# Optimization experiments

Measured on AMD Instinct MI355X. Metric: run time of the kernel, lower is better.

The kernel has to match this reference:

```python
import jax, jax.numpy as jnp
import numpy as np

B, Q, K, D, H = 4, 2048, 2048, 512, 8
DH = D // H
MASK_VAL = -1e6


def setup_inputs() -> dict:
    key = jax.random.key(0)
    ks = jax.random.split(key, 8)
    queries = jax.random.normal(ks[0], (B, Q, D), dtype=jnp.float32)
    keys = jax.random.normal(ks[1], (B, K, D), dtype=jnp.float32)
    values = jax.random.normal(ks[2], (B, K, D), dtype=jnp.float32)
    valid_lens = jax.random.randint(ks[3], (B,), 1, K + 1, dtype=jnp.int32)
    # torch nn.Linear weights: shape [out_features, in_features], y = x @ W.T
    s = 1.0 / np.sqrt(D)
    W_q = jax.random.uniform(ks[4], (D, D), jnp.float32, -s, s)
    W_k = jax.random.uniform(ks[5], (D, D), jnp.float32, -s, s)
    W_v = jax.random.uniform(ks[6], (D, D), jnp.float32, -s, s)
    W_o = jax.random.uniform(ks[7], (D, D), jnp.float32, -s, s)
    return {"queries": queries, "keys": keys, "values": values,
            "valid_lens": valid_lens, "W_q": W_q, "W_k": W_k,
            "W_v": W_v, "W_o": W_o}


def _split_heads(x):
    # [B, S, D] -> [B, H, S, DH]
    b, s, _ = x.shape
    return x.reshape(b, s, H, DH).transpose(0, 2, 1, 3)


def reference(queries, keys, values, valid_lens, W_q, W_k, W_v, W_o):
    q = _split_heads(queries @ W_q.T)   # [B,H,Q,DH]
    k = _split_heads(keys @ W_k.T)      # [B,H,K,DH]
    v = _split_heads(values @ W_v.T)    # [B,H,K,DH]
    scores = jnp.einsum("bhqd,bhkd->bhqk", q, k) / jnp.sqrt(jnp.float32(DH))
    # padding mask: key position < valid_len[b], broadcast over heads & queries
    mask = jnp.arange(K)[None, None, None, :] < valid_lens[:, None, None, None]
    scores = jnp.where(mask, scores, MASK_VAL)
    attn = jax.nn.softmax(scores, axis=-1)  # dropout=eval/no-op
    out = jnp.einsum("bhqk,bhkd->bhqd", attn, v)
    out = out.transpose(0, 2, 1, 3).reshape(queries.shape[0], q.shape[2], D)
    return out @ W_o.T
```

## Files before the change

### kernel.cpp

```cpp
#include <hip/hip_runtime.h>
#include <cstdint>
#include <cstddef>

#define BB  4
#define QQ  2048
#define SK  2048
#define DD  512
#define HH  8
#define DHH 64
#define CS  8
#define ZMAX 4

typedef __bf16 bf16;
typedef bf16  bf16x8 __attribute__((ext_vector_type(8)));
typedef bf16  bf16x4 __attribute__((ext_vector_type(4)));
typedef float f32x4  __attribute__((ext_vector_type(4)));
typedef _Float16 f16;
typedef f16   f16x4 __attribute__((ext_vector_type(4)));
typedef f16   f16x8 __attribute__((ext_vector_type(8)));

__device__ __forceinline__ void async16(void* lds, const void* g) {
  __builtin_amdgcn_global_load_lds(
      (const __attribute__((address_space(1))) unsigned int*)g,
      (__attribute__((address_space(3))) unsigned int*)lds, 16, 0, 0);
}

__device__ __forceinline__ uint32_t pk2(float lo, float hi) {
  return __builtin_amdgcn_perm(__builtin_bit_cast(uint32_t, hi),
                               __builtin_bit_cast(uint32_t, lo), 0x07060302u);
}

__global__ __launch_bounds__(256) void cvt_all(
    const float* __restrict__ q, const float* __restrict__ k,
    const float* __restrict__ v, const float* __restrict__ w0,
    const float* __restrict__ w1, const float* __restrict__ w2,
    const float* __restrict__ w3, bf16* __restrict__ dq,
    bf16* __restrict__ dk, bf16* __restrict__ dv, bf16* __restrict__ dw0,
    bf16* __restrict__ dw1, bf16* __restrict__ dw2, bf16* __restrict__ dw3,
    int nx4, int nw4) {
  const int y = blockIdx.y;
  const float* s;
  bf16* d;
  int n4;
  if (y < 3) {
    n4 = nx4; s = y == 0 ? q : y == 1 ? k : v;
    d = y == 0 ? dq : y == 1 ? dk : dv;
  } else {
    n4 = nw4;
    s = y == 3 ? w0 : y == 4 ? w1 : y == 5 ? w2 : w3;
    d = y == 3 ? dw0 : y == 4 ? dw1 : y == 5 ? dw2 : dw3;
  }
  int i = blockIdx.x * 256 + threadIdx.x;
  if (i < n4) {
    float4 vv = ((const float4*)s)[i];
    bf16x4 o;
    o[0] = (bf16)vv.x; o[1] = (bf16)vv.y; o[2] = (bf16)vv.z; o[3] = (bf16)vv.w;
    ((bf16x4*)d)[i] = o;
  }
}

template <int MT, typename EpiF>
__device__ __forceinline__ void gemm_body(
    const bf16* __restrict__ A, const bf16* __restrict__ B,
    int tM, int tN, EpiF epi_fn) {
  __shared__ __align__(16) bf16 lA[2][MT * 32 * 64];
  __shared__ __align__(16) bf16 lB[2][128 * 64];
  const int tid  = threadIdx.x;
  const int l    = tid & 63;
  const int w    = tid >> 6;
  const int lrow = l & 15, lq = l >> 4;
  const int wm = (w >> 1) * (MT * 16), wn = (w & 1) * 64;

  auto stage = [&](int kt, int buf) {
#pragma unroll
    for (int j = 0; j < MT; ++j) {
      int c = j * 256 + tid, row = c >> 3, gcc = (c & 7) ^ (row & 7);
      async16(&lA[buf][c * 8], &A[(size_t)(tM + row) * DD + kt + gcc * 8]);
    }
#pragma unroll
    for (int j = 0; j < 4; ++j) {
      int c = j * 256 + tid, row = c >> 3, gcc = (c & 7) ^ (row & 7);
      async16(&lB[buf][c * 8], &B[(size_t)(tN + row) * DD + kt + gcc * 8]);
    }
  };

  f32x4 acc[MT][4] = {};
  stage(0, 0);
  for (int it = 0; it < 8; ++it) {
    __syncthreads();
    if (it + 1 < 8) stage((it + 1) * 64, (it + 1) & 1);
    const bf16* bufA = lA[it & 1];
    const bf16* bufB = lB[it & 1];
#pragma unroll
    for (int ks = 0; ks < 2; ++ks) {
      bf16x8 af[MT], bfr[4];
#pragma unroll
      for (int mt = 0; mt < MT; ++mt) {
        int row = wm + mt * 16 + lrow;
        int chunk = row * 8 + ((ks * 4 + lq) ^ (lrow & 7));
        af[mt] = *(const bf16x8*)&bufA[chunk * 8];
      }
#pragma unroll
      for (int nt = 0; nt < 4; ++nt) {
        int row = wn + nt * 16 + lrow;
        int chunk = row * 8 + ((ks * 4 + lq) ^ (lrow & 7));
        bfr[nt] = *(const bf16x8*)&bufB[chunk * 8];
      }
#pragma unroll
      for (int mt = 0; mt < MT; ++mt)
#pragma unroll
        for (int nt = 0; nt < 4; ++nt)
          acc[mt][nt] = __builtin_amdgcn_mfma_f32_16x16x32_bf16(
              af[mt], bfr[nt], acc[mt][nt], 0, 0, 0);
    }
  }

#pragma unroll
  for (int mt = 0; mt < MT; ++mt)
#pragma unroll
    for (int nt = 0; nt < 4; ++nt) {
      int row0 = tM + wm + mt * 16 + lq * 4;
      int col  = tN + wn + nt * 16 + lrow;
      epi_fn(acc[mt][nt], row0, col);
    }
}

__global__ __launch_bounds__(256, 2) void proj3(
    const bf16* __restrict__ xq, const bf16* __restrict__ wq, bf16* __restrict__ qh,
    const bf16* __restrict__ xk, const bf16* __restrict__ wk, bf16* __restrict__ kh,
    const bf16* __restrict__ xv, const bf16* __restrict__ wv, bf16* __restrict__ vt,
    float qscale) {
  const int z = blockIdx.y, x = blockIdx.x;
  if (z < 2) {
    const bf16* A  = z == 0 ? wq : wk;
    const bf16* B  = z == 0 ? xq : xk;
    bf16* Cout     = z == 0 ? qh : kh;
    const float scale = z == 0 ? qscale : 1.0f;
    int tM = (x & 3) * 128, tN = (x >> 2) * 128;
    gemm_body<4>(A, B, tM, tN, [&](const f32x4& a, int row0, int col) {
      int b2 = col >> 11, s = col & 2047;
      int h2 = row0 >> 6, dh0 = row0 & 63;
      bf16x4 o;
#pragma unroll
      for (int r = 0; r < 4; ++r) o[r] = (bf16)(a[r] * scale);
      *(bf16x4*)&Cout[((size_t)(b2 * HH + h2) * QQ + s) * DHH + dh0] = o;
    });
  } else {
    int tM = (x >> 2) * 128, tN = (x & 3) * 128;
    gemm_body<4>(xv, wv, tM, tN, [&](const f32x4& a, int row0, int col) {
      int b2 = row0 >> 11, s0 = row0 & 2047;
      int h2 = col >> 6,  dh = col & 63;
      int tile = s0 >> 6, kk = s0 & 63;
      int g = kk >> 4, a2 = (kk >> 2) & 3;
      int idx0 = ((g >> 1) * 4 + a2) * 8 + (g & 1) * 4;
      bf16x4 o;
#pragma unroll
      for (int r = 0; r < 4; ++r) o[r] = (bf16)a[r];
      *(bf16x4*)&vt[((size_t)(b2 * HH + h2) * DHH + dh) * SK + tile * 64 + idx0] = o;
    });
  }
}

__global__ __launch_bounds__(256, 2) void proj_o(
    const bf16* __restrict__ wo, const bf16* __restrict__ ao,
    float* __restrict__ Cout) {
  const int x = blockIdx.x;
  int tM = (x & 7) * 64, tN = (x >> 3) * 128;
  gemm_body<2>(wo, ao, tM, tN, [&](const f32x4& a, int row0, int col) {
    *(float4*)&Cout[(size_t)col * DD + row0] = *(const float4*)&a;
  });
}

__global__ __launch_bounds__(256, 4) void attn_split(
    const bf16* __restrict__ qh, const bf16* __restrict__ kh,
    const bf16* __restrict__ vt, const int* __restrict__ valid_lens,
    f16* __restrict__ opart, float* __restrict__ lpart) {
  __shared__ __align__(16) bf16 lK[2][64 * 64];
  __shared__ __align__(16) bf16 lV[2][64 * 64];
  const int tid  = threadIdx.x;
  const int l    = tid & 63;
  const int w    = tid >> 6;
  const int lrow = l & 15, lq = l >> 4;
  const int rx   = lrow & 7;
  const int bh = blockIdx.x;
  const int b = bh >> 3;
  const int qt = blockIdx.y, z = blockIdx.z;
  const int vl  = valid_lens[b];
  const int nkt = (vl + 63) >> 6;
  const int kt0 = z * CS;
  const int kt1 = min(nkt, kt0 + CS);
  const size_t pbase = ((size_t)bh * 16 + qt) * ZMAX + z;
  float* lout = lpart + pbase * 128;
  f16*   oout = opart + pbase * 8192;

  if (kt0 >= kt1) {
    if (tid < 128) lout[tid] = 0.f;
    return;
  }

  const int q0 = qt * 128 + w * 32;
  const bf16* qbase = qh + (size_t)bh * QQ * DHH;
  const bf16* kbase = kh + (size_t)bh * SK * DHH;
  const bf16* vbase = vt + (size_t)bh * DHH * SK;

  bf16x8 qf[2][2];
#pragma unroll
  for (int g = 0; g < 2; ++g)
#pragma unroll
    for (int ks = 0; ks < 2; ++ks)
      qf[g][ks] = *(const bf16x8*)
          &qbase[(size_t)(q0 + g * 16 + lrow) * DHH + ks * 32 + lq * 8];

  auto stageKV = [&](int k0, int buf) {
#pragma unroll
    for (int j = 0; j < 2; ++j) {
      int c = j * 256 + tid, row = c >> 3, gcc = (c & 7) ^ (row & 7);
      async16(&lK[buf][c * 8], &kbase[(size_t)(k0 + row) * DHH + gcc * 8]);
    }
#pragma unroll
    for (int j = 0; j < 2; ++j) {
      int c = j * 256 + tid, row = c >> 3, gcc = (c & 7) ^ (row & 7);
      async16(&lV[buf][c * 8], &vbase[(size_t)row * SK + k0 + gcc * 8]);
    }
  };

  f32x4 acc[2][4] = {};
  float rs[2] = {0.f, 0.f};

  stageKV(kt0 * 64, kt0 & 1);
  for (int kt = kt0; kt < kt1; ++kt) {
    __syncthreads();
    if (kt + 1 < kt1) stageKV((kt + 1) * 64, (kt + 1) & 1);
    const bf16* bufK = lK[kt & 1];
    const bf16* bufV = lV[kt & 1];
    const int k0 = kt * 64;

    f32x4 s[2][4] = {};
#pragma unroll
    for (int ks = 0; ks < 2; ++ks) {
#pragma unroll
      for (int t = 0; t < 4; ++t) {
        int row = t * 16 + lrow;
        int chunkc = row * 8 + ((ks * 4 + lq) ^ rx);
        bf16x8 kf = *(const bf16x8*)&bufK[chunkc * 8];
#pragma unroll
        for (int g = 0; g < 2; ++g)
          s[g][t] = __builtin_amdgcn_mfma_f32_16x16x32_bf16(
              kf, qf[g][ks], s[g][t], 0, 0, 0);
      }
    }

    if (vl < k0 + 64) {
#pragma unroll
      for (int t = 0; t < 4; ++t) {
        int kb = k0 + t * 16 + lq * 4;
#pragma unroll
        for (int r = 0; r < 4; ++r)
          if (kb + r >= vl) { s[0][t][r] = -1e30f; s[1][t][r] = -1e30f; }
      }
    }

#pragma unroll
    for (int g = 0; g < 2; ++g)
#pragma unroll
      for (int t = 0; t < 4; ++t)
#pragma unroll
        for (int r = 0; r < 4; ++r) {
          float p = __builtin_amdgcn_exp2f(s[g][t][r]);
          rs[g] += p;
          s[g][t][r] = p;
        }

#pragma unroll
    for (int p2 = 0; p2 < 2; ++p2) {
      union { bf16x8 v; uint32_t u[4]; } pb[2];
#pragma unroll
      for (int g = 0; g < 2; ++g) {
        pb[g].u[0] = pk2(s[g][2 * p2][0], s[g][2 * p2][1]);
        pb[g].u[1] = pk2(s[g][2 * p2][2], s[g][2 * p2][3]);
        pb[g].u[2] = pk2(s[g][2 * p2 + 1][0], s[g][2 * p2 + 1][1]);
        pb[g].u[3] = pk2(s[g][2 * p2 + 1][2], s[g][2 * p2 + 1][3]);
      }
      int cc = (p2 * 4 + lq) ^ rx;
#pragma unroll
      for (int mt = 0; mt < 4; ++mt) {
        int row = mt * 16 + lrow;
        bf16x8 vf = *(const bf16x8*)&bufV[(row * 8 + cc) * 8];
#pragma unroll
        for (int g = 0; g < 2; ++g)
          acc[g][mt] = __builtin_amdgcn_mfma_f32_16x16x32_bf16(
              vf, pb[g].v, acc[g][mt], 0, 0, 0);
      }
    }
  }

#pragma unroll
  for (int g = 0; g < 2; ++g) {
    rs[g] += __shfl_xor(rs[g], 16);
    rs[g] += __shfl_xor(rs[g], 32);
    if (lq == 0) lout[w * 32 + g * 16 + lrow] = rs[g];
  }

#pragma unroll
  for (int g = 0; g < 2; ++g)
#pragma unroll
    for (int mt = 0; mt < 4; ++mt) {
      f16x4 o;
#pragma unroll
      for (int r = 0; r < 4; ++r) o[r] = (f16)acc[g][mt][r];
      *(f16x4*)&oout[(w * 32 + g * 16 + lrow) * 64 + mt * 16 + lq * 4] = o;
    }
}

__global__ __launch_bounds__(256) void attn_combine(
    const f16* __restrict__ opart, const float* __restrict__ lpart,
    bf16* __restrict__ ao) {
  const int bh = blockIdx.x, qt = blockIdx.y;
  const int b = bh >> 3, h = bh & 7;
  const size_t base = ((size_t)bh * 16 + qt) * ZMAX;
  const int t = threadIdx.x, q = t >> 1, ds = (t & 1) * 32;
  float O[32] = {};
  float lsum = 0.f;
#pragma unroll
  for (int z = 0; z < ZMAX; ++z) {
    float lz = lpart[(base + z) * 128 + q];
    if (lz != 0.f) {
      lsum += lz;
      const f16x8* p = (const f16x8*)&opart[(base + z) * 8192 + q * 64 + ds];
#pragma unroll
      for (int j = 0; j < 4; ++j) {
        f16x8 a = p[j];
#pragma unroll
        for (int r = 0; r < 8; ++r) O[j * 8 + r] += (float)a[r];
      }
    }
  }
  float inv = 1.0f / lsum;
  bf16* dst = &ao[((size_t)(b * QQ + qt * 128 + q)) * DD + h * DHH + ds];
#pragma unroll
  for (int j = 0; j < 4; ++j) {
    bf16x8 o;
#pragma unroll
    for (int r = 0; r < 8; ++r) o[r] = (bf16)(O[j * 8 + r] * inv);
    *(bf16x8*)(dst + j * 8) = o;
  }
}

extern "C" void kernel_launch(void* const* d_in, const int* in_sizes, int n_in,
                              void* d_out, int out_size, void* d_ws, size_t ws_size,
                              hipStream_t stream) {
  const float* queries    = (const float*)d_in[0];
  const float* keys       = (const float*)d_in[1];
  const float* values     = (const float*)d_in[2];
  const int*   valid_lens = (const int*)d_in[3];
  const float* W_q = (const float*)d_in[4];
  const float* W_k = (const float*)d_in[5];
  const float* W_v = (const float*)d_in[6];
  const float* W_o = (const float*)d_in[7];

  const size_t NX = (size_t)BB * QQ * DD;
  const size_t NW = (size_t)DD * DD;

  bf16* xq = (bf16*)d_ws;
  bf16* xk = xq + NX;
  bf16* xv = xk + NX;
  bf16* wq = xv + NX;
  bf16* wk = wq + NW;
  bf16* wv = wk + NW;
  bf16* wo = wv + NW;
  bf16* qh = wo + NW;
  bf16* kh = qh + NX;
  bf16* vt = kh + NX;
  f16*  opart = (f16*)(vt + NX);
  float* lpart = (float*)(opart + (size_t)32 * 16 * ZMAX * 8192);
  bf16* ao = xq;

  dim3 blk(256);
  cvt_all<<<dim3(NX / 1024, 7), blk, 0, stream>>>(
      queries, keys, values, W_q, W_k, W_v, W_o,
      xq, xk, xv, wq, wk, wv, wo, (int)(NX / 4), (int)(NW / 4));

  const float qscale = 0.125f * 1.44269504088896340736f;
  proj3<<<dim3(256, 3), blk, 0, stream>>>(xq, wq, qh, xk, wk, kh, xv, wv, vt,
                                          qscale);

  attn_split<<<dim3(BB * HH, QQ / 128, ZMAX), blk, 0, stream>>>(
      qh, kh, vt, valid_lens, opart, lpart);
  attn_combine<<<dim3(BB * HH, QQ / 128), blk, 0, stream>>>(opart, lpart, ao);

  proj_o<<<dim3(512), blk, 0, stream>>>(wo, ao, (float*)d_out);
}
```

Measured before the change: 193.9 us.

## Single-buffer GEMM LDS, raise occupancy, flatten convert grid, halve split-K factor

The GEMM body drops double-buffered LDS staging and uses one buffer with a sync before and after each load, halving LDS use so proj3 and proj_o can declare three blocks per CU. The convert kernel switches from a 2D grid, where most weight-conversion blocks exited early, to a flat 1D grid covering all seven tensors. The attention split factor changes from 4 to 2 with a chunk size of 16, so fewer partials are written and combined. The cost is that global loads no longer overlap MFMA work inside each GEMM block, and attention has less parallelism per query tile.

```diff
diff --git a/kernel.cpp b/kernel.cpp
--- a/kernel.cpp
+++ b/kernel.cpp
@@ -8,8 +8,8 @@
 #define DD  512
 #define HH  8
 #define DHH 64
-#define CS  8
-#define ZMAX 4
+#define CS  16
+#define ZMAX 2
 
 typedef __bf16 bf16;
 typedef bf16  bf16x8 __attribute__((ext_vector_type(8)));
@@ -38,59 +38,55 @@
     bf16* __restrict__ dk, bf16* __restrict__ dv, bf16* __restrict__ dw0,
     bf16* __restrict__ dw1, bf16* __restrict__ dw2, bf16* __restrict__ dw3,
     int nx4, int nw4) {
-  const int y = blockIdx.y;
+  int i = blockIdx.x * 256 + threadIdx.x;
   const float* s;
   bf16* d;
-  int n4;
-  if (y < 3) {
-    n4 = nx4; s = y == 0 ? q : y == 1 ? k : v;
-    d = y == 0 ? dq : y == 1 ? dk : dv;
-  } else {
-    n4 = nw4;
-    s = y == 3 ? w0 : y == 4 ? w1 : y == 5 ? w2 : w3;
-    d = y == 3 ? dw0 : y == 4 ? dw1 : y == 5 ? dw2 : dw3;
-  }
-  int i = blockIdx.x * 256 + threadIdx.x;
-  if (i < n4) {
-    float4 vv = ((const float4*)s)[i];
-    bf16x4 o;
-    o[0] = (bf16)vv.x; o[1] = (bf16)vv.y; o[2] = (bf16)vv.z; o[3] = (bf16)vv.w;
-    ((bf16x4*)d)[i] = o;
-  }
+  if (i < nx4)               { s = q;  d = dq;  }
+  else if (i < 2 * nx4)      { s = k;  d = dk;  i -= nx4; }
+  else if (i < 3 * nx4)      { s = v;  d = dv;  i -= 2 * nx4; }
+  else {
+    int j = i - 3 * nx4;
+    if (j < nw4)             { s = w0; d = dw0; }
+    else if (j < 2 * nw4)    { s = w1; d = dw1; j -= nw4; }
+    else if (j < 3 * nw4)    { s = w2; d = dw2; j -= 2 * nw4; }
+    else if (j < 4 * nw4)    { s = w3; d = dw3; j -= 3 * nw4; }
+    else return;
+    i = j;
+  }
+  float4 vv = ((const float4*)s)[i];
+  bf16x4 o;
+  o[0] = (bf16)vv.x; o[1] = (bf16)vv.y; o[2] = (bf16)vv.z; o[3] = (bf16)vv.w;
+  ((bf16x4*)d)[i] = o;
 }
 
 template <int MT, typename EpiF>
 __device__ __forceinline__ void gemm_body(
     const bf16* __restrict__ A, const bf16* __restrict__ B,
     int tM, int tN, EpiF epi_fn) {
-  __shared__ __align__(16) bf16 lA[2][MT * 32 * 64];
-  __shared__ __align__(16) bf16 lB[2][128 * 64];
+  __shared__ __align__(16) bf16 lA[MT * 32 * 64];
+  __shared__ __align__(16) bf16 lB[128 * 64];
   const int tid  = threadIdx.x;
   const int l    = tid & 63;
   const int w    = tid >> 6;
   const int lrow = l & 15, lq = l >> 4;
   const int wm = (w >> 1) * (MT * 16), wn = (w & 1) * 64;
 
-  auto stage = [&](int kt, int buf) {
+  f32x4 acc[MT][4] = {};
+  for (int it = 0; it < 8; ++it) {
+    const int kt = it * 64;
+    if (it) __syncthreads();
 #pragma unroll
     for (int j = 0; j < MT; ++j) {
       int c = j * 256 + tid, row = c >> 3, gcc = (c & 7) ^ (row & 7);
-      async16(&lA[buf][c * 8], &A[(size_t)(tM + row) * DD + kt + gcc * 8]);
+      async16(&lA[c * 8], &A[(size_t)(tM + row) * DD + kt + gcc * 8]);
     }
 #pragma unroll
     for (int j = 0; j < 4; ++j) {
       int c = j * 256 + tid, row = c >> 3, gcc = (c & 7) ^ (row & 7);
-      async16(&lB[buf][c * 8], &B[(size_t)(tN + row) * DD + kt + gcc * 8]);
-    }
-  };
-
-  f32x4 acc[MT][4] = {};
-  stage(0, 0);
-  for (int it = 0; it < 8; ++it) {
+      async16(&lB[c * 8], &B[(size_t)(tN + row) * DD + kt + gcc * 8]);
+    }
     __syncthreads();
-    if (it + 1 < 8) stage((it + 1) * 64, (it + 1) & 1);
-    const bf16* bufA = lA[it & 1];
-    const bf16* bufB = lB[it & 1];
+
 #pragma unroll
     for (int ks = 0; ks < 2; ++ks) {
       bf16x8 af[MT], bfr[4];
@@ -98,13 +94,13 @@
       for (int mt = 0; mt < MT; ++mt) {
         int row = wm + mt * 16 + lrow;
         int chunk = row * 8 + ((ks * 4 + lq) ^ (lrow & 7));
-        af[mt] = *(const bf16x8*)&bufA[chunk * 8];
+        af[mt] = *(const bf16x8*)&lA[chunk * 8];
       }
 #pragma unroll
       for (int nt = 0; nt < 4; ++nt) {
         int row = wn + nt * 16 + lrow;
         int chunk = row * 8 + ((ks * 4 + lq) ^ (lrow & 7));
-        bfr[nt] = *(const bf16x8*)&bufB[chunk * 8];
+        bfr[nt] = *(const bf16x8*)&lB[chunk * 8];
       }
 #pragma unroll
       for (int mt = 0; mt < MT; ++mt)
@@ -125,7 +121,7 @@
     }
 }
 
-__global__ __launch_bounds__(256, 2) void proj3(
+__global__ __launch_bounds__(256, 3) void proj3(
     const bf16* __restrict__ xq, const bf16* __restrict__ wq, bf16* __restrict__ qh,
     const bf16* __restrict__ xk, const bf16* __restrict__ wk, bf16* __restrict__ kh,
     const bf16* __restrict__ xv, const bf16* __restrict__ wv, bf16* __restrict__ vt,
@@ -161,7 +157,7 @@
   }
 }
 
-__global__ __launch_bounds__(256, 2) void proj_o(
+__global__ __launch_bounds__(256, 3) void proj_o(
     const bf16* __restrict__ wo, const bf16* __restrict__ ao,
     float* __restrict__ Cout) {
   const int x = blockIdx.x;
@@ -376,9 +372,11 @@
   bf16* ao = xq;
 
   dim3 blk(256);
-  cvt_all<<<dim3(NX / 1024, 7), blk, 0, stream>>>(
+  const int nx4 = (int)(NX / 4), nw4 = (int)(NW / 4);
+  const int ncvt = (3 * nx4 + 4 * nw4 + 255) / 256;
+  cvt_all<<<dim3(ncvt), blk, 0, stream>>>(
       queries, keys, values, W_q, W_k, W_v, W_o,
-      xq, xk, xv, wq, wk, wv, wo, (int)(NX / 4), (int)(NW / 4));
+      xq, xk, xv, wq, wk, wv, wo, nx4, nw4);
 
   const float qscale = 0.125f * 1.44269504088896340736f;
   proj3<<<dim3(256, 3), blk, 0, stream>>>(xq, wq, qh, xk, wk, kh, xv, wv, vt,
```

Result: faster. 182.8 us (-5.7%).
